# Kernel optimization log

Hardware: AMD Instinct MI355X
Metric: run time of the kernel (lower is better)

## Reference

```python
import jax, jax.numpy as jnp
import numpy as np

B, S, D, H = 4, 2048, 256, 4
HD = D // H          # head_dim = 64
SPARSITY = 0.1
NH2 = H * H          # 16, distill feature size


def _linear_params(key, out_d, in_d):
    # torch nn.Linear default init: U(-1/sqrt(in), 1/sqrt(in)) for W and b
    limit = 1.0 / np.sqrt(in_d)
    kw, kb = jax.random.split(key)
    W = jax.random.uniform(kw, (out_d, in_d), minval=-limit, maxval=limit, dtype=jnp.float32)
    b = jax.random.uniform(kb, (out_d,), minval=-limit, maxval=limit, dtype=jnp.float32)
    return W, b


def setup_inputs() -> dict:
    key = jax.random.key(0)
    ks = jax.random.split(key, 8)
    x = jax.random.normal(ks[0], (B, S, D), dtype=jnp.float32)
    Wq, bq = _linear_params(ks[1], D, D)
    Wk, bk = _linear_params(ks[2], D, D)
    Wv, bv = _linear_params(ks[3], D, D)
    Wd, bd = _linear_params(ks[4], NH2, NH2)      # distill: 16 -> 16
    Wg, bg = _linear_params(ks[5], NH2, D)        # gate: dim -> 16 (then sigmoid)
    Wgp, bgp = _linear_params(ks[6], D, NH2)      # gate_projection: 16 -> dim
    Wo, bo = _linear_params(ks[7], D, D)          # out: dim -> dim
    return dict(x=x, Wq=Wq, bq=bq, Wk=Wk, bk=bk, Wv=Wv, bv=bv,
                Wd=Wd, bd=bd, Wg=Wg, bg=bg, Wgp=Wgp, bgp=bgp, Wo=Wo, bo=bo)


def reference(x, Wq, bq, Wk, bk, Wv, bv, Wd, bd, Wg, bg, Wgp, bgp, Wo, bo):
    b, s, d = x.shape
    scale = HD ** -0.5
    # QKV projections, split into heads: [b, h, s, hd]
    Q = (x @ Wq.T + bq).reshape(b, s, H, HD).transpose(0, 2, 1, 3)
    K = (x @ Wk.T + bk).reshape(b, s, H, HD).transpose(0, 2, 1, 3)
    V = (x @ Wv.T + bv).reshape(b, s, H, HD).transpose(0, 2, 1, 3)
    scores = jnp.einsum('bhqd,bhkd->bhqk', Q, K) * scale  # [b,h,s,s]
    # per-row quantile threshold (torch.quantile linear interpolation == jnp default)
    q = 1.0 - SPARSITY  # 0.9
    thr = jnp.quantile(scores, q, axis=-1, keepdims=True)
    masked = jnp.where(scores >= thr, scores, -jnp.inf)
    probs = jax.nn.softmax(masked, axis=-1)
    att = jnp.einsum('bhqk,bhkd->bhqd', probs, V)
    att = att.transpose(0, 2, 1, 3).reshape(b, s, d)  # [b,s,dim]
    # distill: view as (-1, 16) -> Linear(16,16) -> view back
    distilled = (att.reshape(-1, NH2) @ Wd.T + bd).reshape(b, s, d)
    # gate from mean-pooled input
    g = jax.nn.sigmoid(x.mean(axis=1) @ Wg.T + bg)  # [b,16]
    g = (g @ Wgp.T + bgp)[:, None, :]               # [b,1,dim] broadcast over seq
    mixed = g * distilled + (1.0 - g) * att
    return mixed @ Wo.T + bo
```

## Files before the change

### kernel.cpp

```cpp
#include <hip/hip_runtime.h>
#include <hip/hip_bf16.h>
#include <math.h>


#define CAP 128

typedef __attribute__((ext_vector_type(8))) short short8;
typedef __attribute__((ext_vector_type(4))) float floatx4;
typedef _Float16 half8 __attribute__((ext_vector_type(8)));
typedef _Float16 half4v __attribute__((ext_vector_type(4)));
#define MFMA16(a,b,c) __builtin_amdgcn_mfma_f32_16x16x32_bf16(a,b,c,0,0,0)
#define MFMAH(a,b,c)  __builtin_amdgcn_mfma_f32_16x16x32_f16(a,b,c,0,0,0)

__device__ __forceinline__ float umt(unsigned u){
  return __uint_as_float((u & 0x80000000u) ? (u & 0x7fffffffu) : ~u);
}
__device__ __forceinline__ float wmin_f(float v){
  #pragma unroll
  for (int m=1;m<64;m<<=1) v = fminf(v, __shfl_xor(v,m,64));
  return v;
}
__device__ __forceinline__ int mbcnt64(unsigned long long m){
  return (int)__builtin_amdgcn_mbcnt_hi((unsigned)(m>>32),
         __builtin_amdgcn_mbcnt_lo((unsigned)(m & 0xffffffffull), 0u));
}
__device__ __forceinline__ short8 ldb8(const __hip_bfloat16* p){
  return *(const short8*)p;
}
__device__ __forceinline__ void cvt8(short* dh, short* dl, float4 v0, float4 v1){
  const float vv[8] = {v0.x,v0.y,v0.z,v0.w,v1.x,v1.y,v1.z,v1.w};
  short8 h8, l8;
  #pragma unroll
  for (int i=0;i<8;i++){
    const __hip_bfloat16 h = __float2bfloat16(vv[i]);
    const __hip_bfloat16 l = __float2bfloat16(vv[i] - __bfloat162float(h));
    h8[i] = *(const short*)&h;
    l8[i] = *(const short*)&l;
  }
  *(short8*)dh = h8;
  *(short8*)dl = l8;
}

#define FULLSEL(SU, PSTART, V206, V205)                                        \
  {                                                                            \
    unsigned v = (PSTART);                                                     \
    _Pragma("unroll 1")                                                        \
    for (int bit = 19; bit >= 0; --bit){                                       \
      const float cf = umt(v | (1u << bit));                                   \
      int n = 0;                                                               \
      _Pragma("unroll")                                                        \
      for (int i = 0; i < 32; i++) n += (int)__popcll(__ballot(SU[i] >= cf));  \
      if (n >= 206) v |= (1u << bit);                                          \
    }                                                                          \
    V206 = umt(v);                                                             \
    int cgt = 0; float mn = 3.0e38f;                                           \
    _Pragma("unroll")                                                          \
    for (int i = 0; i < 32; i++){                                              \
      const float u = SU[i];                                                   \
      const bool gt = (u > V206);                                              \
      cgt += (int)__popcll(__ballot(gt));                                      \
      mn = (gt && u < mn) ? u : mn;                                            \
    }                                                                          \
    mn = wmin_f(mn);                                                           \
    V205 = (cgt == 205) ? mn : V206;                                           \
  }

__global__ void xpart_kernel(const float* __restrict__ x, float* __restrict__ xpart){
  const int ch = blockIdx.x, b = blockIdx.y, t = threadIdx.x;
  const float* xp = x + ((size_t)b*2048 + (size_t)ch*16)*256 + t;
  float s = 0.f;
  #pragma unroll
  for (int i=0;i<16;i++) s += xp[(size_t)i*256];
  xpart[(size_t)(b*128+ch)*256 + t] = s;
}

__global__ void gate_kernel(const float* __restrict__ xpart,
                            const float* __restrict__ Wg, const float* __restrict__ bg,
                            const float* __restrict__ Wgp,const float* __restrict__ bgp,
                            float* __restrict__ gate_ws){
  __shared__ float xm[256];
  __shared__ float part[16][17];
  __shared__ float g16[16];
  const int t = threadIdx.x;
  const int b = blockIdx.x;
  float s = 0.f;
  for (int ch=0; ch<128; ch++) s += xpart[(size_t)(b*128+ch)*256 + t];
  xm[t] = s * (1.0f/2048.0f);
  __syncthreads();
  {
    const int j = t >> 4, dg = t & 15;
    float p = 0.f;
    #pragma unroll
    for (int d=0; d<16; d++) p = fmaf(xm[dg*16+d], Wg[j*256 + dg*16 + d], p);
    part[j][dg] = p;
  }
  __syncthreads();
  if (t < 16){
    float z = bg[t];
    #pragma unroll
    for (int g=0; g<16; g++) z += part[t][g];
    g16[t] = 1.0f/(1.0f + __expf(-z));
  }
  __syncthreads();
  float z2 = bgp[t];
  #pragma unroll
  for (int j=0;j<16;j++) z2 = fmaf(g16[j], Wgp[t*16+j], z2);
  gate_ws[b*256 + t] = z2;
}

__global__ __launch_bounds__(256) void qkv_gemm(
    const float* __restrict__ x,
    const float* __restrict__ Wq, const float* __restrict__ bq,
    const float* __restrict__ Wk, const float* __restrict__ bk,
    const float* __restrict__ Wv, const float* __restrict__ bv,
    __hip_bfloat16* __restrict__ qh, __hip_bfloat16* __restrict__ ql,
    __hip_bfloat16* __restrict__ kh, __hip_bfloat16* __restrict__ kl,
    _Float16* __restrict__ vth, _Float16* __restrict__ vtl){
  __shared__ short Ah[64][40], Al[64][40];
  __shared__ short Bh[64][40], Bl[64][40];
  const int m0 = blockIdx.x * 64;
  const int n0g = blockIdx.y * 64;
  const int sect = n0g >> 8;
  const int nl0 = n0g & 255;
  const float* W    = (sect==0) ? Wq : ((sect==1) ? Wk : Wv);
  const float* bias = (sect==0) ? bq : ((sect==1) ? bk : bv);
  const int tid = threadIdx.x;
  const int lr = tid >> 2, lc = tid & 3;
  const int w = tid >> 6, ln = tid & 63;
  const int lm = ln & 15, lk = (ln >> 4) * 8;

  floatx4 acc[4];
  #pragma unroll
  for (int tl=0;tl<4;tl++) acc[tl] = (floatx4){0.f,0.f,0.f,0.f};

  for (int k0 = 0; k0 < 256; k0 += 32){
    const float4 a0 = *(const float4*)&x[(size_t)(m0 +lr)*256 + k0 + lc*8];
    const float4 a1 = *(const float4*)&x[(size_t)(m0 +lr)*256 + k0 + lc*8 + 4];
    const float4 b0 = *(const float4*)&W[(size_t)(nl0+lr)*256 + k0 + lc*8];
    const float4 b1 = *(const float4*)&W[(size_t)(nl0+lr)*256 + k0 + lc*8 + 4];
    __syncthreads();
    cvt8(&Ah[lr][lc*8], &Al[lr][lc*8], a0, a1);
    cvt8(&Bh[lr][lc*8], &Bl[lr][lc*8], b0, b1);
    __syncthreads();
    const short8 ah8 = *(const short8*)&Ah[w*16+lm][lk];
    const short8 al8 = *(const short8*)&Al[w*16+lm][lk];
    #pragma unroll
    for (int tl = 0; tl < 4; tl++){
      const short8 bh8 = *(const short8*)&Bh[tl*16+lm][lk];
      const short8 bl8 = *(const short8*)&Bl[tl*16+lm][lk];
      acc[tl] = MFMA16(ah8, bh8, acc[tl]);
      acc[tl] = MFMA16(al8, bh8, acc[tl]);
      acc[tl] = MFMA16(ah8, bl8, acc[tl]);
      acc[tl] = MFMA16(al8, bl8, acc[tl]);
    }
  }

  #pragma unroll
  for (int tl = 0; tl < 4; tl++){
    const int f = nl0 + tl*16 + lm;
    const int hh = f >> 6, hd = f & 63;
    const float bf = bias[f];
    if (sect == 2){
      const int mB = m0 + w*16 + (ln >> 4)*4;
      const int bidx = mB >> 11, s0 = mB & 2047;
      half4v hv, lv;
      #pragma unroll
      for (int i=0;i<4;i++){
        const float val = acc[tl][i] + bf;
        const _Float16 hx = (_Float16)val;
        hv[i] = hx;
        lv[i] = (_Float16)(val - (float)hx);
      }
      const size_t row = (size_t)((bidx*4+hh)*64 + hd);
      *(half4v*)(vth + row*2048 + s0) = hv;
      *(half4v*)(vtl + row*2048 + s0) = lv;
    } else {
      #pragma unroll
      for (int i=0;i<4;i++){
        const int m = m0 + w*16 + (ln >> 4)*4 + i;
        const int bidx = m >> 11, s = m & 2047;
        const float val = acc[tl][i] + bf;
        const size_t idx = (size_t)((bidx*4+hh)*2048 + s)*64 + hd;
        const __hip_bfloat16 hi = __float2bfloat16(val);
        const float lo = val - __bfloat162float(hi);
        if (sect == 0){ qh[idx] = hi; ql[idx] = __float2bfloat16(lo); }
        else          { kh[idx] = hi; kl[idx] = __float2bfloat16(lo); }
      }
    }
  }
}

__global__ __launch_bounds__(512, 4) void attn_kernel(
    const __hip_bfloat16* __restrict__ qh, const __hip_bfloat16* __restrict__ ql,
    const __hip_bfloat16* __restrict__ kh, const __hip_bfloat16* __restrict__ kl,
    const _Float16* __restrict__ vth, const _Float16* __restrict__ vtl,
    const float* __restrict__ Wd, const float* __restrict__ bd,
    const float* __restrict__ gate_ws, float* __restrict__ mix_ws){
  __shared__ __align__(16) char smem[74240];
  __shared__ float obuf[16][66];
  __shared__ float zbuf[16];

  float (*buf0)[516] = (float (*)[516])smem;
  float (*buf1)[516] = (float (*)[516])(smem + 33024);

  const int bh = blockIdx.y;
  const int q0 = blockIdx.x * 16;
  const int tid = threadIdx.x;
  const int w = tid >> 6, ln = tid & 63;
  const int lm = ln & 15;
  const int lk = (ln >> 4) * 8;
  const int qa = 2*w, qb = 2*w + 1;

  const __hip_bfloat16* Qh = qh + ((size_t)bh*2048 + q0)*64;
  const __hip_bfloat16* Ql = ql + ((size_t)bh*2048 + q0)*64;
  const __hip_bfloat16* Kh = kh + ((size_t)bh*2048 + w*256)*64;
  const __hip_bfloat16* Kl = kl + ((size_t)bh*2048 + w*256)*64;

  float su0[32], su1[32];

  #pragma unroll
  for (int c = 0; c < 4; c++){
    float (*bufc)[516] = (c & 1) ? buf1 : buf0;
    const short8 ah0 = ldb8(Qh + lm*64 + lk);
    const short8 ah1 = ldb8(Qh + lm*64 + 32 + lk);
    const short8 al0 = ldb8(Ql + lm*64 + lk);
    const short8 al1 = ldb8(Ql + lm*64 + 32 + lk);
    floatx4 acc[4];
    #pragma unroll
    for (int tl = 0; tl < 4; tl++){
      const int krow = c*64 + tl*16 + lm;
      short8 bh0 = ldb8(Kh + krow*64 + lk);
      short8 bh1 = ldb8(Kh + krow*64 + 32 + lk);
      short8 bl0 = ldb8(Kl + krow*64 + lk);
      short8 bl1 = ldb8(Kl + krow*64 + 32 + lk);
      floatx4 a = {0.f,0.f,0.f,0.f};
      a = MFMA16(ah0, bh0, a);
      a = MFMA16(ah1, bh1, a);
      a = MFMA16(al0, bh0, a);
      a = MFMA16(al1, bh1, a);
      a = MFMA16(ah0, bl0, a);
      a = MFMA16(ah1, bl1, a);
      a = MFMA16(al0, bl0, a);
      a = MFMA16(al1, bl1, a);
      acc[tl] = a;
    }
    const int wr = (ln >> 4) * 4;
    #pragma unroll
    for (int tl = 0; tl < 4; tl++){
      const int col = w*64 + tl*16 + lm;
      bufc[wr+0][col] = acc[tl].x * 0.125f;
      bufc[wr+1][col] = acc[tl].y * 0.125f;
      bufc[wr+2][col] = acc[tl].z * 0.125f;
      bufc[wr+3][col] = acc[tl].w * 0.125f;
    }
    __syncthreads();
    float4 ra0 = *(const float4*)&bufc[qa][4*ln];
    float4 ra1 = *(const float4*)&bufc[qa][256 + 4*ln];
    float4 rb0 = *(const float4*)&bufc[qb][4*ln];
    float4 rb1 = *(const float4*)&bufc[qb][256 + 4*ln];
    const int o = c*8;
    su0[o+0]=ra0.x; su0[o+1]=ra0.y; su0[o+2]=ra0.z; su0[o+3]=ra0.w;
    su0[o+4]=ra1.x; su0[o+5]=ra1.y; su0[o+6]=ra1.z; su0[o+7]=ra1.w;
    su1[o+0]=rb0.x; su1[o+1]=rb0.y; su1[o+2]=rb0.z; su1[o+3]=rb0.w;
    su1[o+4]=rb1.x; su1[o+5]=rb1.y; su1[o+6]=rb1.z; su1[o+7]=rb1.w;
  }
  __syncthreads();

  unsigned p0 = 0, p1 = 0;
  #pragma unroll 1
  for (int bit = 31; bit >= 20; --bit){
    const float c0f = umt(p0 | (1u << bit));
    const float c1f = umt(p1 | (1u << bit));
    int v0 = 0, n1 = 0;
    #pragma unroll
    for (int i = 0; i < 32; i++){
      v0 += (su0[i] >= c0f) ? 1 : 0;
      n1 += (int)__popcll(__ballot(su1[i] >= c1f));
    }
    #pragma unroll
    for (int m=1;m<64;m<<=1) v0 += __shfl_xor(v0,m,64);
    p0 |= (v0 >= 206) ? (1u << bit) : 0u;
    if (n1 >= 206) p1 |= (1u << bit);
  }

  const int b = bh >> 2, h = bh & 3;

  const float pf0  = umt(p0),             pf1  = umt(p1);
  const float hif0 = umt(p0 + 0x100000u), hif1 = umt(p1 + 0x100000u);
  float* cand0 = (float*)(smem + 65536 + (size_t)(2*w + 0)*512);
  float* cand1 = (float*)(smem + 65536 + (size_t)(2*w + 1)*512);

  int above0 = 0, nc0 = 0, above1 = 0, nc1 = 0;
  float mx0 = -3.0e38f, mx1 = -3.0e38f, mnab0 = 3.0e38f, mnab1 = 3.0e38f;
  #pragma unroll
  for (int i = 0; i < 32; i++){
    const float u0 = su0[i], u1 = su1[i];
    mx0 = fmaxf(mx0, u0);
    mx1 = fmaxf(mx1, u1);
    const bool ab0 = (u0 >= hif0), ab1 = (u1 >= hif1);
    above0 += ab0 ? 1 : 0;
    above1 += ab1 ? 1 : 0;
    if (ab0) mnab0 = fminf(mnab0, u0);
    if (ab1) mnab1 = fminf(mnab1, u1);
    const bool cd0 = (u0 >= pf0) && !ab0, cd1 = (u1 >= pf1) && !ab1;
    const unsigned long long bal0 = __ballot(cd0);
    if (cd0){
      const int pos = nc0 + mbcnt64(bal0);
      if (pos < CAP) cand0[pos] = u0;
    }
    nc0 += (int)__popcll(bal0);
    const unsigned long long bal1 = __ballot(cd1);
    if (cd1){
      const int pos = nc1 + mbcnt64(bal1);
      if (pos < CAP) cand1[pos] = u1;
    }
    nc1 += (int)__popcll(bal1);
  }
  int ab01 = above0 | (above1 << 16);
  #pragma unroll
  for (int m=1;m<64;m<<=1){
    ab01  += __shfl_xor(ab01, m,64);
    mx0   = fmaxf(mx0,   __shfl_xor(mx0,  m,64));
    mx1   = fmaxf(mx1,   __shfl_xor(mx1,  m,64));
    mnab0 = fminf(mnab0, __shfl_xor(mnab0,m,64));
    mnab1 = fminf(mnab1, __shfl_xor(mnab1,m,64));
  }
  above0 = ab01 & 0xffff;
  above1 = ab01 >> 16;

  float v206_0, v205_0, v206_1, v205_1;
  if (__builtin_expect(nc0 <= CAP && nc1 <= CAP, 1)){
    const int j0 = 206 - above0, j1 = 206 - above1;
    const float cv00 = (ln      < nc0) ? cand0[ln]      : -3.0e38f;
    const float cv01 = (ln + 64 < nc0) ? cand0[ln + 64] : -3.0e38f;
    const float cv10 = (ln      < nc1) ? cand1[ln]      : -3.0e38f;
    const float cv11 = (ln + 64 < nc1) ? cand1[ln + 64] : -3.0e38f;
    unsigned v0 = p0, v1 = p1;
    #pragma unroll 1
    for (int bit = 19; bit >= 0; --bit){
      const float cf0 = umt(v0 | (1u << bit));
      const float cf1 = umt(v1 | (1u << bit));
      const int n0 = (int)__popcll(__ballot(cv00 >= cf0))
                   + (int)__popcll(__ballot(cv01 >= cf0));
      const int n1 = (int)__popcll(__ballot(cv10 >= cf1))
                   + (int)__popcll(__ballot(cv11 >= cf1));
      if (n0 >= j0) v0 |= (1u << bit);
      if (n1 >= j1) v1 |= (1u << bit);
    }
    v206_0 = umt(v0);
    v206_1 = umt(v1);
    const int cgtc0 = (int)__popcll(__ballot(cv00 > v206_0))
                    + (int)__popcll(__ballot(cv01 > v206_0));
    const int cgtc1 = (int)__popcll(__ballot(cv10 > v206_1))
                    + (int)__popcll(__ballot(cv11 > v206_1));
    float mnc0 = 3.0e38f, mnc1 = 3.0e38f;
    if (cv00 > v206_0) mnc0 = fminf(mnc0, cv00);
    if (cv01 > v206_0) mnc0 = fminf(mnc0, cv01);
    if (cv10 > v206_1) mnc1 = fminf(mnc1, cv10);
    if (cv11 > v206_1) mnc1 = fminf(mnc1, cv11);
    #pragma unroll
    for (int m=1;m<64;m<<=1){
      mnc0 = fminf(mnc0, __shfl_xor(mnc0,m,64));
      mnc1 = fminf(mnc1, __shfl_xor(mnc1,m,64));
    }
    const int cgt0 = above0 + cgtc0, cgt1 = above1 + cgtc1;
    v205_0 = (cgt0 == 205) ? ((cgtc0 > 0) ? mnc0 : mnab0) : v206_0;
    v205_1 = (cgt1 == 205) ? ((cgtc1 > 0) ? mnc1 : mnab1) : v206_1;
  } else {
    FULLSEL(su0, p0, v206_0, v205_0);
    FULLSEL(su1, p1, v206_1, v205_1);
  }

  const float thr0 = (float)((double)v206_0 + 0.3*((double)v205_0 - (double)v206_0));
  const float thr1 = (float)((double)v206_1 + 0.3*((double)v205_1 - (double)v206_1));

  float zl0 = 0.f, zl1 = 0.f;
  char* rba = smem + (size_t)qa*4096 + ((size_t)(ln >> 4) << 9)
            + (size_t)((((ln & 15) << 3)) ^ ((qa & 7) << 4));
  char* rbb = smem + (size_t)qb*4096 + ((size_t)(ln >> 4) << 9)
            + (size_t)((((ln & 15) << 3)) ^ ((qb & 7) << 4));
  #pragma unroll
  for (int c = 0; c < 4; c++){
    #pragma unroll
    for (int h4 = 0; h4 < 2; h4++){
      half4v pk0, pk1;
      #pragma unroll
      for (int jj = 0; jj < 4; jj++){
        const int i = c*8 + h4*4 + jj;
        const float s0 = su0[i], s1 = su1[i];
        const float pr0 = (s0 >= thr0) ? __expf(s0 - mx0) : 0.f;
        const float pr1 = (s1 >= thr1) ? __expf(s1 - mx1) : 0.f;
        const _Float16 ph0 = (_Float16)pr0;
        const _Float16 ph1 = (_Float16)pr1;
        zl0 += (float)ph0;
        zl1 += (float)ph1;
        pk0[jj] = ph0;
        pk1[jj] = ph1;
      }
      *(half4v*)(rba + h4*2048 + c*128) = pk0;
      *(half4v*)(rbb + h4*2048 + c*128) = pk1;
    }
  }
  #pragma unroll
  for (int m=1;m<64;m<<=1){
    zl0 += __shfl_xor(zl0,m,64);
    zl1 += __shfl_xor(zl1,m,64);
  }
  if (ln == 0){ zbuf[qa] = 1.0f / zl0; zbuf[qb] = 1.0f / zl1; }

  __syncthreads();

  const int ct = w & 3, kh2 = w >> 2;
  const int arow = ln & 15;
  const int sw = (arow & 7) << 4;
  const char* prow = smem + (size_t)arow*4096;
  const int klog0 = (kh2 << 11) + ((ln >> 4) << 4);
  const _Float16* vhp = vth + ((size_t)bh*64 + ct*16 + arow)*2048 + (kh2 << 10) + ((ln >> 4) << 3);
  const _Float16* vlp = vtl + ((size_t)bh*64 + ct*16 + arow)*2048 + (kh2 << 10) + ((ln >> 4) << 3);

  floatx4 acch = {0.f,0.f,0.f,0.f};
  floatx4 accl = {0.f,0.f,0.f,0.f};
  #pragma unroll 4
  for (int kk = 0; kk < 32; kk++){
    const half8 a   = *(const half8*)(prow + ((klog0 + kk*64) ^ sw));
    const half8 vh8 = *(const half8*)(vhp + kk*32);
    const half8 vl8 = *(const half8*)(vlp + kk*32);
    acch = MFMAH(a, vh8, acch);
    accl = MFMAH(a, vl8, accl);
  }
  floatx4 acc = acch + accl;

  float gt = 0.f, bda = 0.f;
  float wdv[16];
  if (kh2 == 1){
    const int r0 = (ln >> 4) * 4;
    #pragma unroll
    for (int i = 0; i < 4; i++) obuf[r0+i][ct*16 + arow] = acc[i];
  } else {
    gt  = gate_ws[(size_t)b*256 + h*64 + ct*16 + arow];
    bda = bd[arow];
    #pragma unroll
    for (int m4 = 0; m4 < 4; m4++){
      const float4 t4 = *(const float4*)&Wd[arow*16 + m4*4];
      wdv[m4*4+0]=t4.x; wdv[m4*4+1]=t4.y; wdv[m4*4+2]=t4.z; wdv[m4*4+3]=t4.w;
    }
  }
  __syncthreads();
  if (kh2 == 0){
    const int r0 = (ln >> 4) * 4;
    const int gb = ln & 48;
    #pragma unroll
    for (int i = 0; i < 4; i++){
      const int r = r0 + i;
      const float o = (acc[i] + obuf[r][ct*16 + arow]) * zbuf[r];
      float d = bda;
      #pragma unroll
      for (int m = 0; m < 16; m++)
        d = fmaf(__shfl(o, gb + m, 64), wdv[m], d);
      const float mixed = gt*d + (1.0f - gt)*o;
      mix_ws[(size_t)(b*2048 + q0 + r)*256 + h*64 + ct*16 + arow] = mixed;
    }
  }
}

__global__ __launch_bounds__(256) void out_gemm(
    const float* __restrict__ A, const float* __restrict__ Wo,
    const float* __restrict__ bo, float* __restrict__ out){
  __shared__ short Ah[64][40], Al[64][40];
  __shared__ short Bh[64][40], Bl[64][40];
  const int m0 = blockIdx.x * 64;
  const int n0 = blockIdx.y * 64;
  const int tid = threadIdx.x;
  const int lr = tid >> 2, lc = tid & 3;
  const int w = tid >> 6, ln = tid & 63;
  const int lm = ln & 15, lk = (ln >> 4) * 8;

  floatx4 acc[4];
  #pragma unroll
  for (int tl=0;tl<4;tl++) acc[tl] = (floatx4){0.f,0.f,0.f,0.f};

  for (int k0 = 0; k0 < 256; k0 += 32){
    const float4 a0 = *(const float4*)&A [(size_t)(m0+lr)*256 + k0 + lc*8];
    const float4 a1 = *(const float4*)&A [(size_t)(m0+lr)*256 + k0 + lc*8 + 4];
    const float4 b0 = *(const float4*)&Wo[(size_t)(n0+lr)*256 + k0 + lc*8];
    const float4 b1 = *(const float4*)&Wo[(size_t)(n0+lr)*256 + k0 + lc*8 + 4];
    __syncthreads();
    cvt8(&Ah[lr][lc*8], &Al[lr][lc*8], a0, a1);
    cvt8(&Bh[lr][lc*8], &Bl[lr][lc*8], b0, b1);
    __syncthreads();
    const short8 ah8 = *(const short8*)&Ah[w*16+lm][lk];
    const short8 al8 = *(const short8*)&Al[w*16+lm][lk];
    #pragma unroll
    for (int tl = 0; tl < 4; tl++){
      const short8 bh8 = *(const short8*)&Bh[tl*16+lm][lk];
      const short8 bl8 = *(const short8*)&Bl[tl*16+lm][lk];
      acc[tl] = MFMA16(ah8, bh8, acc[tl]);
      acc[tl] = MFMA16(al8, bh8, acc[tl]);
      acc[tl] = MFMA16(ah8, bl8, acc[tl]);
      acc[tl] = MFMA16(al8, bl8, acc[tl]);
    }
  }

  #pragma unroll
  for (int tl = 0; tl < 4; tl++){
    const int f = n0 + tl*16 + lm;
    const float bf = bo[f];
    #pragma unroll
    for (int i=0;i<4;i++){
      const int m = m0 + w*16 + (ln >> 4)*4 + i;
      out[(size_t)m*256 + f] = acc[tl][i] + bf;
    }
  }
}

extern "C" void kernel_launch(void* const* d_in, const int* in_sizes, int n_in,
                              void* d_out, int out_size, void* d_ws, size_t ws_size,
                              hipStream_t stream) {
  const float* x   = (const float*)d_in[0];
  const float* Wq  = (const float*)d_in[1];  const float* bq  = (const float*)d_in[2];
  const float* Wk  = (const float*)d_in[3];  const float* bk  = (const float*)d_in[4];
  const float* Wv  = (const float*)d_in[5];  const float* bv  = (const float*)d_in[6];
  const float* Wd  = (const float*)d_in[7];  const float* bd  = (const float*)d_in[8];
  const float* Wg  = (const float*)d_in[9];  const float* bg  = (const float*)d_in[10];
  const float* Wgp = (const float*)d_in[11]; const float* bgp = (const float*)d_in[12];
  const float* Wo  = (const float*)d_in[13]; const float* bo  = (const float*)d_in[14];

  char* base = (char*)d_ws;
  float* mix_ws = (float*)(base);
  __hip_bfloat16* qh = (__hip_bfloat16*)(base + (size_t)( 8<<20));
  __hip_bfloat16* ql = (__hip_bfloat16*)(base + (size_t)(12<<20));
  __hip_bfloat16* kh = (__hip_bfloat16*)(base + (size_t)(16<<20));
  __hip_bfloat16* kl = (__hip_bfloat16*)(base + (size_t)(20<<20));
  _Float16* vth = (_Float16*)(base + (size_t)(24<<20));
  _Float16* vtl = (_Float16*)(base + (size_t)(28<<20));
  float* xpart  = (float*)(base + (size_t)(32<<20));
  float* gate_ws= (float*)(base + (size_t)(33<<20));

  xpart_kernel<<<dim3(128,4), 256, 0, stream>>>(x, xpart);
  gate_kernel<<<4, 256, 0, stream>>>(xpart, Wg, bg, Wgp, bgp, gate_ws);
  qkv_gemm<<<dim3(128,12), 256, 0, stream>>>(x, Wq,bq, Wk,bk, Wv,bv,
                                             qh, ql, kh, kl, vth, vtl);
  attn_kernel<<<dim3(128,16), 512, 0, stream>>>(qh, ql, kh, kl, vth, vtl,
                                                Wd, bd, gate_ws, mix_ws);
  out_gemm<<<dim3(128,4), 256, 0, stream>>>(mix_ws, Wo, bo, (float*)d_out);
}
```

Baseline: 415.7 us.

## Halve attention kernel LDS footprint by single-buffering scores and splitting PV into halves

Shared memory drops from about 74KB plus extras to about 37KB. The double-buffered score staging becomes a single buffer guarded by an extra barrier, and the probability tile is written and consumed in two key halves of 1024 columns each, reusing the same region. The Q fragment loads are also hoisted out of the chunk loop. The aim is to let more 512-thread blocks fit per CU, improving occupancy, at the cost of additional __syncthreads per block.

Measured after the change: 405.8 us. 2.4% less time.

```diff
diff --git a/kernel.cpp b/kernel.cpp
--- a/kernel.cpp
+++ b/kernel.cpp
@@ -196,12 +196,10 @@
     const _Float16* __restrict__ vth, const _Float16* __restrict__ vtl,
     const float* __restrict__ Wd, const float* __restrict__ bd,
     const float* __restrict__ gate_ws, float* __restrict__ mix_ws){
-  __shared__ __align__(16) char smem[74240];
-  __shared__ float obuf[16][66];
-  __shared__ float zbuf[16];
-
-  float (*buf0)[516] = (float (*)[516])smem;
-  float (*buf1)[516] = (float (*)[516])(smem + 33024);
+  __shared__ __align__(16) char smem[37312];
+  float (*buf)[516] = (float (*)[516])smem;
+  float (*obuf)[66] = (float (*)[66])(smem + 33024);
+  float* zbuf = (float*)(smem + 37248);
 
   const int bh = blockIdx.y;
   const int q0 = blockIdx.x * 16;
@@ -218,13 +216,13 @@
 
   float su0[32], su1[32];
 
+  const short8 ah0 = ldb8(Qh + lm*64 + lk);
+  const short8 ah1 = ldb8(Qh + lm*64 + 32 + lk);
+  const short8 al0 = ldb8(Ql + lm*64 + lk);
+  const short8 al1 = ldb8(Ql + lm*64 + 32 + lk);
+
   #pragma unroll
   for (int c = 0; c < 4; c++){
-    float (*bufc)[516] = (c & 1) ? buf1 : buf0;
-    const short8 ah0 = ldb8(Qh + lm*64 + lk);
-    const short8 ah1 = ldb8(Qh + lm*64 + 32 + lk);
-    const short8 al0 = ldb8(Ql + lm*64 + lk);
-    const short8 al1 = ldb8(Ql + lm*64 + 32 + lk);
     floatx4 acc[4];
     #pragma unroll
     for (int tl = 0; tl < 4; tl++){
@@ -244,20 +242,21 @@
       a = MFMA16(al1, bl1, a);
       acc[tl] = a;
     }
+    __syncthreads();
     const int wr = (ln >> 4) * 4;
     #pragma unroll
     for (int tl = 0; tl < 4; tl++){
       const int col = w*64 + tl*16 + lm;
-      bufc[wr+0][col] = acc[tl].x * 0.125f;
-      bufc[wr+1][col] = acc[tl].y * 0.125f;
-      bufc[wr+2][col] = acc[tl].z * 0.125f;
-      bufc[wr+3][col] = acc[tl].w * 0.125f;
-    }
-    __syncthreads();
-    float4 ra0 = *(const float4*)&bufc[qa][4*ln];
-    float4 ra1 = *(const float4*)&bufc[qa][256 + 4*ln];
-    float4 rb0 = *(const float4*)&bufc[qb][4*ln];
-    float4 rb1 = *(const float4*)&bufc[qb][256 + 4*ln];
+      buf[wr+0][col] = acc[tl].x * 0.125f;
+      buf[wr+1][col] = acc[tl].y * 0.125f;
+      buf[wr+2][col] = acc[tl].z * 0.125f;
+      buf[wr+3][col] = acc[tl].w * 0.125f;
+    }
+    __syncthreads();
+    float4 ra0 = *(const float4*)&buf[qa][4*ln];
+    float4 ra1 = *(const float4*)&buf[qa][256 + 4*ln];
+    float4 rb0 = *(const float4*)&buf[qb][4*ln];
+    float4 rb1 = *(const float4*)&buf[qb][256 + 4*ln];
     const int o = c*8;
     su0[o+0]=ra0.x; su0[o+1]=ra0.y; su0[o+2]=ra0.z; su0[o+3]=ra0.w;
     su0[o+4]=ra1.x; su0[o+5]=ra1.y; su0[o+6]=ra1.z; su0[o+7]=ra1.w;
@@ -287,8 +286,8 @@
 
   const float pf0  = umt(p0),             pf1  = umt(p1);
   const float hif0 = umt(p0 + 0x100000u), hif1 = umt(p1 + 0x100000u);
-  float* cand0 = (float*)(smem + 65536 + (size_t)(2*w + 0)*512);
-  float* cand1 = (float*)(smem + 65536 + (size_t)(2*w + 1)*512);
+  float* cand0 = (float*)(smem + (size_t)w*1024);
+  float* cand1 = (float*)(smem + (size_t)w*1024 + 512);
 
   int above0 = 0, nc0 = 0, above1 = 0, nc1 = 0;
   float mx0 = -3.0e38f, mx1 = -3.0e38f, mnab0 = 3.0e38f, mnab1 = 3.0e38f;
@@ -374,19 +373,30 @@
   const float thr0 = (float)((double)v206_0 + 0.3*((double)v205_0 - (double)v206_0));
   const float thr1 = (float)((double)v206_1 + 0.3*((double)v205_1 - (double)v206_1));
 
+  __syncthreads();
+
   float zl0 = 0.f, zl1 = 0.f;
-  char* rba = smem + (size_t)qa*4096 + ((size_t)(ln >> 4) << 9)
+  char* rba = smem + (size_t)qa*2048 + ((size_t)(ln >> 4) << 9)
             + (size_t)((((ln & 15) << 3)) ^ ((qa & 7) << 4));
-  char* rbb = smem + (size_t)qb*4096 + ((size_t)(ln >> 4) << 9)
+  char* rbb = smem + (size_t)qb*2048 + ((size_t)(ln >> 4) << 9)
             + (size_t)((((ln & 15) << 3)) ^ ((qb & 7) << 4));
-  #pragma unroll
-  for (int c = 0; c < 4; c++){
-    #pragma unroll
-    for (int h4 = 0; h4 < 2; h4++){
+
+  const int ct = w & 3, khq = w >> 2;
+  const int arow = ln & 15;
+  const int sw = (arow & 7) << 4;
+  const char* prow = smem + (size_t)arow*2048;
+  const int klog0 = (khq << 10) + ((ln >> 4) << 4);
+  floatx4 acch = {0.f,0.f,0.f,0.f};
+  floatx4 accl = {0.f,0.f,0.f,0.f};
+
+  #pragma unroll
+  for (int hp = 0; hp < 2; hp++){
+    #pragma unroll
+    for (int c = 0; c < 4; c++){
       half4v pk0, pk1;
       #pragma unroll
       for (int jj = 0; jj < 4; jj++){
-        const int i = c*8 + h4*4 + jj;
+        const int i = c*8 + hp*4 + jj;
         const float s0 = su0[i], s1 = su1[i];
         const float pr0 = (s0 >= thr0) ? __expf(s0 - mx0) : 0.f;
         const float pr1 = (s1 >= thr1) ? __expf(s1 - mx1) : 0.f;
@@ -397,42 +407,38 @@
         pk0[jj] = ph0;
         pk1[jj] = ph1;
       }
-      *(half4v*)(rba + h4*2048 + c*128) = pk0;
-      *(half4v*)(rbb + h4*2048 + c*128) = pk1;
-    }
-  }
-  #pragma unroll
-  for (int m=1;m<64;m<<=1){
-    zl0 += __shfl_xor(zl0,m,64);
-    zl1 += __shfl_xor(zl1,m,64);
-  }
-  if (ln == 0){ zbuf[qa] = 1.0f / zl0; zbuf[qb] = 1.0f / zl1; }
-
-  __syncthreads();
-
-  const int ct = w & 3, kh2 = w >> 2;
-  const int arow = ln & 15;
-  const int sw = (arow & 7) << 4;
-  const char* prow = smem + (size_t)arow*4096;
-  const int klog0 = (kh2 << 11) + ((ln >> 4) << 4);
-  const _Float16* vhp = vth + ((size_t)bh*64 + ct*16 + arow)*2048 + (kh2 << 10) + ((ln >> 4) << 3);
-  const _Float16* vlp = vtl + ((size_t)bh*64 + ct*16 + arow)*2048 + (kh2 << 10) + ((ln >> 4) << 3);
-
-  floatx4 acch = {0.f,0.f,0.f,0.f};
-  floatx4 accl = {0.f,0.f,0.f,0.f};
-  #pragma unroll 4
-  for (int kk = 0; kk < 32; kk++){
-    const half8 a   = *(const half8*)(prow + ((klog0 + kk*64) ^ sw));
-    const half8 vh8 = *(const half8*)(vhp + kk*32);
-    const half8 vl8 = *(const half8*)(vlp + kk*32);
-    acch = MFMAH(a, vh8, acch);
-    accl = MFMAH(a, vl8, accl);
+      *(half4v*)(rba + c*128) = pk0;
+      *(half4v*)(rbb + c*128) = pk1;
+    }
+    if (hp == 1){
+      #pragma unroll
+      for (int m=1;m<64;m<<=1){
+        zl0 += __shfl_xor(zl0,m,64);
+        zl1 += __shfl_xor(zl1,m,64);
+      }
+      if (ln == 0){ zbuf[qa] = 1.0f / zl0; zbuf[qb] = 1.0f / zl1; }
+    }
+    __syncthreads();
+
+    const _Float16* vhp_ = vth + ((size_t)bh*64 + ct*16 + arow)*2048
+                         + (hp << 10) + (khq << 9) + ((ln >> 4) << 3);
+    const _Float16* vlp_ = vtl + ((size_t)bh*64 + ct*16 + arow)*2048
+                         + (hp << 10) + (khq << 9) + ((ln >> 4) << 3);
+    #pragma unroll 4
+    for (int kk = 0; kk < 16; kk++){
+      const half8 a   = *(const half8*)(prow + ((klog0 + kk*64) ^ sw));
+      const half8 vh8 = *(const half8*)(vhp_ + kk*32);
+      const half8 vl8 = *(const half8*)(vlp_ + kk*32);
+      acch = MFMAH(a, vh8, acch);
+      accl = MFMAH(a, vl8, accl);
+    }
+    if (hp == 0) __syncthreads();
   }
   floatx4 acc = acch + accl;
 
   float gt = 0.f, bda = 0.f;
   float wdv[16];
-  if (kh2 == 1){
+  if (khq == 1){
     const int r0 = (ln >> 4) * 4;
     #pragma unroll
     for (int i = 0; i < 4; i++) obuf[r0+i][ct*16 + arow] = acc[i];
@@ -446,7 +452,7 @@
     }
   }
   __syncthreads();
-  if (kh2 == 0){
+  if (khq == 0){
     const int r0 = (ln >> 4) * 4;
     const int gb = ln & 48;
     #pragma unroll
```
